# Optimization experiments

Measured on AMD Instinct MI355X. Metric: run time of the kernel, lower is better.

## Reference

```python
import jax, jax.numpy as jnp
import numpy as np

N, E, B = 10000, 160000, 16
IN, H, A, L, OUT = 16, 64, 8, 2, 1
MSG_IN = 2 * (H + 1) + 1   # 131 = concat(x_i, x_j, additional_message_features)
UPD_IN = H + 1 + H         # 129 = concat(x_aug, aggregated message)


def _tp(h, a, W, b):
    # scalar-irreps fully-connected O3 tensor product == bilinear map + bias
    return jnp.einsum('ni,nj,ijk->nk', h, a, W) + b


def setup_inputs() -> dict:
    key = jax.random.key(0)
    ks = jax.random.split(key, 24)
    f32 = jnp.float32
    def rn(k, shape, scale=1.0):
        return jax.random.normal(k, shape, f32) * scale
    def w(k, shape):
        fan = shape[-3] * shape[-2]
        return rn(k, shape, 1.0 / np.sqrt(fan))
    return {
        'x': rn(ks[0], (N, IN)),
        'edge_index': jax.random.randint(ks[1], (2, E), 0, N),
        'edge_attr': rn(ks[2], (E, A)),
        'node_attr': rn(ks[3], (N, A)),
        'additional_message_features': rn(ks[4], (E, 1)),
        'additional_node_features': rn(ks[5], (N, 1)),
        'batch': jnp.sort(jax.random.randint(ks[6], (N,), 0, B)),
        'W_emb': w(ks[7], (IN + 1, A, H)), 'b_emb': jnp.zeros((H,), f32),
        'Wm1': w(ks[8], (L, MSG_IN, A, H)), 'bm1': jnp.zeros((L, H), f32),
        'Wm2': w(ks[9], (L, H, A, H)), 'bm2': jnp.zeros((L, H), f32),
        'Wu1': w(ks[10], (L, UPD_IN, A, H)), 'bu1': jnp.zeros((L, H), f32),
        'Wu2': w(ks[11], (L, H, A, H)), 'bu2': jnp.zeros((L, H), f32),
        'Wp1': w(ks[12], (H, A, H)), 'bp1': jnp.zeros((H,), f32),
        'Wp2': w(ks[13], (H, A, H)), 'bp2': jnp.zeros((H,), f32),
        'Wq1': rn(ks[14], (H, H), 1.0 / np.sqrt(H)), 'bq1': jnp.zeros((H,), f32),
        'Wq2': rn(ks[15], (H, OUT), 1.0 / np.sqrt(H)), 'bq2': jnp.zeros((OUT,), f32),
    }


def _forward(x, edge_attr, node_attr, amf, anf,
             W_emb, b_emb, Wm1, bm1, Wm2, bm2, Wu1, bu1, Wu2, bu2,
             Wp1, bp1, Wp2, bp2, Wq1, bq1, Wq2, bq2, edge_index, batch):
    silu = jax.nn.silu
    src, dst = edge_index[0], edge_index[1]  # source_to_target: aggregate at dst
    n = x.shape[0]
    # embedding: concat additional node features, bilinear TP with node_attr
    h = _tp(jnp.concatenate([x, anf], -1), node_attr, W_emb, b_emb)          # [N,H]
    for l in range(Wm1.shape[0]):  # loop over structurally distinct layers
        h_aug = jnp.concatenate([h, anf], -1)                                # [N,H+1]
        m_in = jnp.concatenate([h_aug[dst], h_aug[src], amf], -1)            # [E,MSG_IN]
        m = silu(_tp(m_in, edge_attr, Wm1[l], bm1[l]))                       # TP + swish gate
        m = silu(_tp(m, edge_attr, Wm2[l], bm2[l]))                          # sg2=True -> gated too
        agg = jax.ops.segment_sum(m, dst, num_segments=n)                    # scatter-add [N,H]
        u = silu(_tp(jnp.concatenate([h_aug, agg], -1), node_attr, Wu1[l], bu1[l]))
        u = _tp(u, node_attr, Wu2[l], bu2[l])                                # no gate on 2nd TP
        h = h + u                                                            # residual, adnid stripped
    # pre-pool MLP (SwishGate TP then plain TP)
    p = silu(_tp(h, node_attr, Wp1, bp1))
    p = _tp(p, node_attr, Wp2, bp2)                                          # [N,POOL=H]
    # global mean pool over graphs
    counts = jax.ops.segment_sum(jnp.ones((n,), p.dtype), batch, num_segments=B)
    g = jax.ops.segment_sum(p, batch, num_segments=B) / jnp.maximum(counts, 1.0)[:, None]
    # post-pool: TP with trivial 1x0e attr == plain linear
    g = silu(g @ Wq1 + bq1)
    return g @ Wq2 + bq2                                                     # [B,OUT]


def reference(x, edge_index, edge_attr, node_attr, additional_message_features,
              additional_node_features, batch, W_emb, b_emb, Wm1, bm1, Wm2, bm2,
              Wu1, bu1, Wu2, bu2, Wp1, bp1, Wp2, bp2, Wq1, bq1, Wq2, bq2):
    return _forward(x, edge_attr, node_attr, additional_message_features,
                    additional_node_features, W_emb, b_emb, Wm1, bm1, Wm2, bm2,
                    Wu1, bu1, Wu2, bu2, Wp1, bp1, Wp2, bp2, Wq1, bq1, Wq2, bq2,
                    edge_index, batch)
```

## Files before the change

kernel.cpp:

```cpp
#include <hip/hip_runtime.h>
#include <hip/hip_bf16.h>
#include <math.h>

constexpr int N = 10000;
constexpr int E = 160000;
constexpr int B = 16;
constexpr int POOL_CHUNKS = 80;
constexpr int MS = 72;
constexpr int HS = 96;

typedef short bf16x8 __attribute__((ext_vector_type(8)));
typedef short bf16x4 __attribute__((ext_vector_type(4)));
typedef float f32x4 __attribute__((ext_vector_type(4)));

__device__ __forceinline__ float silu_f(float x) {
    return x / (1.0f + __expf(-x));
}
__device__ __forceinline__ float bf2f(short s) {
    union { unsigned u; float f; } c; c.u = (unsigned)(unsigned short)s << 16; return c.f;
}

__device__ __forceinline__ void w2_body(
        int idx, const float* __restrict__ Wsrc,
        __hip_bfloat16* __restrict__ Whi, __hip_bfloat16* __restrict__ Wlo) {
    int l = idx >> 15;
    int rem = idx & 32767;
    int kk = rem >> 11;
    int nt = (rem >> 9) & 3;
    int c  = (rem >> 5) & 15;
    int q  = (rem >> 3) & 3;
    int j  = rem & 7;
    int i = q * 16 + kk;
    int k = nt * 16 + c;
    float wv = Wsrc[(size_t)l * 32768 + i * 512 + j * 64 + k];
    __hip_bfloat16 hi = __float2bfloat16(wv);
    Whi[idx] = hi;
    Wlo[idx] = __float2bfloat16(wv - __bfloat162float(hi));
}

__device__ __forceinline__ void w2h_body(
        int idx, const float* __restrict__ Wsrc, __hip_bfloat16* __restrict__ Whi) {
    int l = idx >> 15;
    int rem = idx & 32767;
    int kk = rem >> 11;
    int nt = (rem >> 9) & 3;
    int c  = (rem >> 5) & 15;
    int q  = (rem >> 3) & 3;
    int j  = rem & 7;
    int i = q * 16 + kk;
    int k = nt * 16 + c;
    Whi[idx] = __float2bfloat16(Wsrc[(size_t)l * 32768 + i * 512 + j * 64 + k]);
}

__device__ __forceinline__ void wu1_body(
        int idx, const float* __restrict__ Wu1,
        __hip_bfloat16* __restrict__ Whi, __hip_bfloat16* __restrict__ Wlo) {
    int l = idx / 67584;
    int rem = idx % 67584;
    int kk = rem / 2048;
    int r2 = rem % 2048;
    int nt = (r2 >> 9) & 3;
    int c  = (r2 >> 5) & 15;
    int q  = (r2 >> 3) & 3;
    int j  = r2 & 7;
    int i = q * 33 + kk;
    float wv = (i < 129) ? Wu1[(size_t)l * 129 * 512 + i * 512 + j * 64 + nt * 16 + c] : 0.f;
    __hip_bfloat16 hi = __float2bfloat16(wv);
    Whi[idx] = hi;
    Wlo[idx] = __float2bfloat16(wv - __bfloat162float(hi));
}

__device__ __forceinline__ void wm1z_body(
        int idx, const float* __restrict__ Wm1, __hip_bfloat16* __restrict__ Whi) {
    int l = idx / 71680;
    int rem = idx % 71680;
    int kkn = rem >> 9;
    int off = rem & 511;
    int kk = kkn >> 2;
    int nt = kkn & 3;
    int c16 = off >> 5;
    int q = (off >> 3) & 3;
    int j = off & 7;
    int k = nt * 16 + c16;
    int wi = -1;
    if (kk < 17) { int i = q * 17 + kk; if (i <= 64) wi = i; }
    else if (kk < 34) { int s = q * 17 + (kk - 17); if (s <= 64) wi = 65 + s; }
    else { if (q == 0) wi = 130; }
    float wv = (wi >= 0) ? Wm1[((size_t)l * 131 + wi) * 512 + j * 64 + k] : 0.f;
    Whi[idx] = __float2bfloat16(wv);
}

constexpr int PB_W2H  = 0;
constexpr int PB_WM1Z = PB_W2H  + 256;
constexpr int PB_WU1  = PB_WM1Z + 560;
constexpr int PB_WU2  = PB_WU1  + 528;
constexpr int PB_WP1  = PB_WU2  + 256;
constexpr int PB_WP2  = PB_WP1  + 128;
constexpr int PB_ZERO = PB_WP2  + 128;
constexpr int PB_EMB  = PB_ZERO + 40;
constexpr int PB_TOTAL= PB_EMB  + 625;

__global__ __launch_bounds__(256) void k_pre(
        const float* __restrict__ Wm2, __hip_bfloat16* __restrict__ W2hi,
        const float* __restrict__ Wm1, __hip_bfloat16* __restrict__ Wm1zhi,
        const float* __restrict__ Wu1w, __hip_bfloat16* __restrict__ Wu1hi, __hip_bfloat16* __restrict__ Wu1lo,
        const float* __restrict__ Wu2w, __hip_bfloat16* __restrict__ Wu2hi, __hip_bfloat16* __restrict__ Wu2lo,
        const float* __restrict__ Wp1w, __hip_bfloat16* __restrict__ Wp1hi, __hip_bfloat16* __restrict__ Wp1lo,
        const float* __restrict__ Wp2w, __hip_bfloat16* __restrict__ Wp2hi, __hip_bfloat16* __restrict__ Wp2lo,
        int* __restrict__ hist,
        const float* __restrict__ x, const float* __restrict__ anf,
        const float* __restrict__ na, const float* __restrict__ W_emb,
        const float* __restrict__ b_emb,
        float* __restrict__ h, __hip_bfloat16* __restrict__ hb, float* __restrict__ agg) {
    __shared__ float xs[16][18];
    __shared__ float na_s[16][8];
    int tid = threadIdx.x;
    int bx = blockIdx.x;
    if (bx < PB_WM1Z) {
        w2h_body((bx - PB_W2H) * 256 + tid, Wm2, W2hi);
    } else if (bx < PB_WU1) {
        wm1z_body((bx - PB_WM1Z) * 256 + tid, Wm1, Wm1zhi);
    } else if (bx < PB_WU2) {
        wu1_body((bx - PB_WU1) * 256 + tid, Wu1w, Wu1hi, Wu1lo);
    } else if (bx < PB_WP1) {
        w2_body((bx - PB_WU2) * 256 + tid, Wu2w, Wu2hi, Wu2lo);
    } else if (bx < PB_WP2) {
        w2_body((bx - PB_WP1) * 256 + tid, Wp1w, Wp1hi, Wp1lo);
    } else if (bx < PB_ZERO) {
        w2_body((bx - PB_WP2) * 256 + tid, Wp2w, Wp2hi, Wp2lo);
    } else if (bx < PB_EMB) {
        int i = (bx - PB_ZERO) * 256 + tid;
        if (i < N) hist[i] = 0;
    } else {
        int eb = bx - PB_EMB;
        int w = tid >> 6, l = tid & 63;
        int n0 = eb * 16;
        {
            int r = tid >> 4, c = tid & 15;
            xs[r][c] = x[(size_t)(n0 + r) * 16 + c];
        }
        if (tid < 16) xs[tid][16] = anf[n0 + tid];
        if (tid < 128) na_s[tid >> 3][tid & 7] = na[(size_t)n0 * 8 + tid];
        float4 z4 = {0.f, 0.f, 0.f, 0.f};
        ((float4*)(agg + (size_t)eb * 1024))[tid] = z4;
        for (int t = tid; t < 192; t += 256)
            ((float4*)(hb + (size_t)n0 * HS))[t] = z4;
        __syncthreads();
        float acc[4];
#pragma unroll
        for (int t = 0; t < 4; ++t) acc[t] = b_emb[l];
        for (int i = 0; i < 17; ++i) {
#pragma unroll
            for (int j = 0; j < 8; ++j) {
                float wv = W_emb[(i * 8 + j) * 64 + l];
#pragma unroll
                for (int t = 0; t < 4; ++t) {
                    int nn = w * 4 + t;
                    acc[t] = fmaf(xs[nn][i] * na_s[nn][j], wv, acc[t]);
                }
            }
        }
        int slot = (l / 17) * 24 + l % 17;
#pragma unroll
        for (int t = 0; t < 4; ++t) {
            int n = n0 + w * 4 + t;
            h[(size_t)n * 64 + l] = acc[t];
            hb[(size_t)n * HS + slot] = __float2bfloat16(acc[t]);
        }
        if (tid < 16) hb[(size_t)(n0 + tid) * HS + 85] = __float2bfloat16(xs[tid][16]);
    }
}

__global__ __launch_bounds__(256) void k_hist(
        const int* __restrict__ eidx, int* __restrict__ hist) {
    int e = blockIdx.x * 256 + threadIdx.x;
    if (e < E) atomicAdd(&hist[eidx[E + e]], 1);
}

__global__ __launch_bounds__(1024) void k_scan(
        const int* __restrict__ hist, int* __restrict__ cursor) {
    __shared__ int wsum[16];
    int t = threadIdx.x;
    int base = t * 10;
    int loc[10];
    int s = 0;
#pragma unroll
    for (int i = 0; i < 10; ++i) {
        int v = (base + i < N) ? hist[base + i] : 0;
        loc[i] = s;
        s += v;
    }
    int lane = t & 63, w = t >> 6;
    int incl = s;
    for (int off = 1; off < 64; off <<= 1) {
        int u = __shfl_up(incl, off, 64);
        if (lane >= off) incl += u;
    }
    if (lane == 63) wsum[w] = incl;
    __syncthreads();
    if (t == 0) {
        int a = 0;
        for (int i2 = 0; i2 < 16; ++i2) { int v = wsum[i2]; wsum[i2] = a; a += v; }
    }
    __syncthreads();
    int excl = incl - s + wsum[w];
#pragma unroll
    for (int i = 0; i < 10; ++i) {
        int p = base + i;
        if (p < N) cursor[p] = excl + loc[i];
    }
}

__global__ __launch_bounds__(256) void k_scatter_sort(
        const int* __restrict__ eidx, const float* __restrict__ ea,
        const float* __restrict__ amf, int* __restrict__ cursor,
        int* __restrict__ dstS, float4* __restrict__ recs) {
    int e = blockIdx.x * 256 + threadIdx.x;
    if (e < E) {
        int d = eidx[E + e];
        int p = atomicAdd(&cursor[d], 1);
        dstS[p] = d;
        float4 a0 = ((const float4*)ea)[(size_t)e * 2];
        float4 a1 = ((const float4*)ea)[(size_t)e * 2 + 1];
        float4 r0 = {__int_as_float(eidx[e]), amf[e], a0.x, a0.y};
        float4 r1 = {a0.z, a0.w, a1.x, a1.y};
        float4 r2 = {a1.z, a1.w, 0.f, 0.f};
        recs[(size_t)p * 3 + 0] = r0;
        recs[(size_t)p * 3 + 1] = r1;
        recs[(size_t)p * 3 + 2] = r2;
    }
}

__device__ __forceinline__ void zgemm_stage(
        const __hip_bfloat16* xsrc, int xstride, int kkmax, int Lq,
        int w, int c16, int q, int lofs, const float* naA,
        const __hip_bfloat16* __restrict__ Whi, const __hip_bfloat16* __restrict__ Wlo,
        float (*part_s)[16][64]) {
    f32x4 zero4 = {0.f, 0.f, 0.f, 0.f};
    f32x4 acc[4];
#pragma unroll
    for (int nt = 0; nt < 4; ++nt) acc[nt] = zero4;
    for (int kk = w; kk < kkmax; kk += 4) {
        bf16x8 bh[4], bl[4];
#pragma unroll
        for (int nt = 0; nt < 4; ++nt) {
            int off = (kk * 4 + nt) * 512 + lofs;
            bh[nt] = *(const bf16x8*)(Whi + off);
            bl[nt] = *(const bf16x8*)(Wlo + off);
        }
        float mv = __bfloat162float(xsrc[c16 * xstride + q * Lq + kk]);
        union { bf16x8 v; __hip_bfloat16 hx[8]; } au;
#pragma unroll
        for (int j = 0; j < 8; ++j) au.hx[j] = __float2bfloat16(mv * naA[j]);
#pragma unroll
        for (int nt = 0; nt < 4; ++nt) {
            acc[nt] = __builtin_amdgcn_mfma_f32_16x16x32_bf16(au.v, bh[nt], acc[nt], 0, 0, 0);
            acc[nt] = __builtin_amdgcn_mfma_f32_16x16x32_bf16(au.v, bl[nt], acc[nt], 0, 0, 0);
        }
    }
#pragma unroll
    for (int nt = 0; nt < 4; ++nt)
#pragma unroll
        for (int r = 0; r < 4; ++r) part_s[w][q * 4 + r][nt * 16 + c16] = acc[nt][r];
}

__global__ __launch_bounds__(256, 4) void k_edge(
        const float4* __restrict__ recs, const int* __restrict__ dstS,
        const __hip_bfloat16* __restrict__ hb,
        const __hip_bfloat16* __restrict__ W1hi, const float* __restrict__ bm1_l,
        const __hip_bfloat16* __restrict__ W2hi,
        const float* __restrict__ bm2_l, float* __restrict__ agg) {
    __shared__ __align__(16) char smem_u[4 * 4608];
    __shared__ int dst_s[128];
    int tid = threadIdx.x;
    int l = tid & 63, w = tid >> 6;
    int e0 = blockIdx.x * 128;
    __hip_bfloat16* m_s = (__hip_bfloat16*)(smem_u + w * 4608);
    float* m2 = (float*)(smem_u + w * 4608);

    if (l < 32) dst_s[w * 32 + l] = dstS[e0 + w * 32 + l];

    int c16 = l & 15, q = l >> 4;
    int e0w = w * 32;
    float eaA[2][8], amfA[2];
    int dL[2], sL[2];
#pragma unroll
    for (int mt = 0; mt < 2; ++mt) {
        int e = e0 + e0w + mt * 16 + c16;
        float4 r0 = recs[(size_t)e * 3];
        float4 r1 = recs[(size_t)e * 3 + 1];
        float4 r2 = recs[(size_t)e * 3 + 2];
        sL[mt] = __float_as_int(r0.x);
        amfA[mt] = r0.y;
        eaA[mt][0] = r0.z; eaA[mt][1] = r0.w;
        eaA[mt][2] = r1.x; eaA[mt][3] = r1.y; eaA[mt][4] = r1.z; eaA[mt][5] = r1.w;
        eaA[mt][6] = r2.x; eaA[mt][7] = r2.y;
        dL[mt] = dstS[e];
    }
    float bR1[4], bR2[4];
#pragma unroll
    for (int nt = 0; nt < 4; ++nt) {
        bR1[nt] = bm1_l[nt * 16 + c16];
        bR2[nt] = bm2_l[nt * 16 + c16];
    }
    int lofs = (c16 * 4 + q) * 8;
    f32x4 zero4 = {0.f, 0.f, 0.f, 0.f};

    bf16x4 xD[2][5], xS[2][5];
#pragma unroll
    for (int mt = 0; mt < 2; ++mt) {
        const __hip_bfloat16* bd = hb + (size_t)dL[mt] * HS + q * 24;
        const __hip_bfloat16* bs = hb + (size_t)sL[mt] * HS + q * 24;
#pragma unroll
        for (int t = 0; t < 5; ++t) {
            xD[mt][t] = *(const bf16x4*)(bd + t * 4);
            xS[mt][t] = *(const bf16x4*)(bs + t * 4);
        }
    }

    f32x4 acc1[2][4];
#pragma unroll
    for (int mt = 0; mt < 2; ++mt)
#pragma unroll
        for (int nt = 0; nt < 4; ++nt) acc1[mt][nt] = zero4;
    {
        bf16x8 bhr[3][4];
#pragma unroll
        for (int u = 0; u < 2; ++u)
#pragma unroll
            for (int nt = 0; nt < 4; ++nt)
                bhr[u][nt] = *(const bf16x8*)(W1hi + (u * 4 + nt) * 512 + lofs);
#pragma unroll
        for (int u = 0; u < 35; ++u) {
            if (u + 2 < 35) {
#pragma unroll
                for (int nt = 0; nt < 4; ++nt)
                    bhr[(u + 2) % 3][nt] = *(const bf16x8*)(W1hi + ((u + 2) * 4 + nt) * 512 + lofs);
            }
#pragma unroll
            for (int mt = 0; mt < 2; ++mt) {
                float xv;
                if (u < 17)       xv = bf2f(xD[mt][u >> 2][u & 3]);
                else if (u < 34)  { int s = u - 17; xv = bf2f(xS[mt][s >> 2][s & 3]); }
                else              xv = (q == 0) ? amfA[mt] : 0.f;
                union { bf16x8 v; __hip_bfloat16 hx[8]; } au;
#pragma unroll
                for (int j = 0; j < 8; ++j) au.hx[j] = __float2bfloat16(xv * eaA[mt][j]);
#pragma unroll
                for (int nt = 0; nt < 4; ++nt)
                    acc1[mt][nt] = __builtin_amdgcn_mfma_f32_16x16x32_bf16(au.v, bhr[u % 3][nt], acc1[mt][nt], 0, 0, 0);
            }
            if ((u & 7) == 7 && u < 34) __syncthreads();
        }
    }
#pragma unroll
    for (int mt = 0; mt < 2; ++mt)
#pragma unroll
        for (int nt = 0; nt < 4; ++nt) {
            int kd = nt * 16 + c16;
            float bias = bR1[nt];
#pragma unroll
            for (int r = 0; r < 4; ++r) {
                int el = mt * 16 + q * 4 + r;
                m_s[el * MS + kd] = __float2bfloat16(silu_f(bias + acc1[mt][nt][r]));
            }
        }

    bf16x4 mR[2][4];
#pragma unroll
    for (int mt = 0; mt < 2; ++mt)
#pragma unroll
        for (int t = 0; t < 4; ++t)
            mR[mt][t] = *(const bf16x4*)&m_s[(mt * 16 + c16) * MS + q * 16 + t * 4];

    asm volatile("" ::: "memory");

    f32x4 acc[2][4];
#pragma unroll
    for (int mt = 0; mt < 2; ++mt)
#pragma unroll
        for (int nt = 0; nt < 4; ++nt) acc[mt][nt] = zero4;
    {
        bf16x8 bhr[3][4];
#pragma unroll
        for (int u = 0; u < 2; ++u)
#pragma unroll
            for (int nt = 0; nt < 4; ++nt)
                bhr[u][nt] = *(const bf16x8*)(W2hi + (u * 4 + nt) * 512 + lofs);
#pragma unroll
        for (int kk = 0; kk < 16; ++kk) {
            if (kk + 2 < 16) {
#pragma unroll
                for (int nt = 0; nt < 4; ++nt)
                    bhr[(kk + 2) % 3][nt] = *(const bf16x8*)(W2hi + ((kk + 2) * 4 + nt) * 512 + lofs);
            }
#pragma unroll
            for (int mt = 0; mt < 2; ++mt) {
                float mv = bf2f(mR[mt][kk >> 2][kk & 3]);
                union { bf16x8 v; __hip_bfloat16 h[8]; } au;
#pragma unroll
                for (int j = 0; j < 8; ++j) au.h[j] = __float2bfloat16(mv * eaA[mt][j]);
#pragma unroll
                for (int nt = 0; nt < 4; ++nt)
                    acc[mt][nt] = __builtin_amdgcn_mfma_f32_16x16x32_bf16(au.v, bhr[kk % 3][nt], acc[mt][nt], 0, 0, 0);
            }
            if (kk == 7) __syncthreads();
        }
    }

#pragma unroll
    for (int mt = 0; mt < 2; ++mt) {
#pragma unroll
        for (int nt = 0; nt < 4; ++nt) {
            int kd = nt * 16 + c16;
            float bias = bR2[nt];
#pragma unroll
            for (int r = 0; r < 4; ++r)
                m2[(q * 4 + r) * 66 + kd] = silu_f(bias + acc[mt][nt][r]);
        }
        int rb = w * 32 + mt * 16;
        float run = 0.f;
        int cur_d = dst_s[rb];
        for (int i = 0; i < 16; ++i) {
            int d = dst_s[rb + i];
            if (d != cur_d) {
                atomicAdd(&agg[(size_t)cur_d * 64 + l], run);
                run = 0.f;
                cur_d = d;
            }
            run += m2[i * 66 + l];
        }
        atomicAdd(&agg[(size_t)cur_d * 64 + l], run);
        asm volatile("" ::: "memory");
    }
}

__global__ __launch_bounds__(256) void k_upd_hb(
        const float* __restrict__ h_in, const float* __restrict__ anf,
        const float* __restrict__ na, const float* __restrict__ agg_in,
        const __hip_bfloat16* __restrict__ W1hi, const __hip_bfloat16* __restrict__ W1lo,
        const float* __restrict__ bu1_l,
        const __hip_bfloat16* __restrict__ W2hi_, const __hip_bfloat16* __restrict__ W2lo_,
        const float* __restrict__ bu2_l,
        float* __restrict__ h, __hip_bfloat16* __restrict__ hb, float* __restrict__ agg) {
    __shared__ __align__(16) __hip_bfloat16 xa_s[16 * 136];
    __shared__ __align__(16) __hip_bfloat16 u1_s[16 * 72];
    __shared__ float part_s[4][16][64];
    int tid = threadIdx.x;
    int w = tid >> 6, l = tid & 63;
    int n0 = blockIdx.x * 16;
    for (int idx = tid; idx < 16 * 132; idx += 256) {
        int r = idx / 132, c = idx % 132;
        int n = n0 + r;
        float v;
        if (c < 64) v = h_in[(size_t)n * 64 + c];
        else if (c == 64) v = anf[n];
        else if (c < 129) v = agg_in[(size_t)n * 64 + (c - 65)];
        else v = 0.f;
        xa_s[r * 136 + c] = __float2bfloat16(v);
    }
    int c16 = l & 15, q = l >> 4;
    float naA[8];
#pragma unroll
    for (int j = 0; j < 8; ++j) naA[j] = na[(size_t)(n0 + c16) * 8 + j];
    __syncthreads();
    float4 z4 = {0.f, 0.f, 0.f, 0.f};
    ((float4*)(agg + (size_t)blockIdx.x * 1024))[tid] = z4;
    for (int t = tid; t < 192; t += 256)
        ((float4*)(hb + (size_t)n0 * HS))[t] = z4;
    int lofs = (c16 * 4 + q) * 8;
    zgemm_stage(xa_s, 136, 33, 33, w, c16, q, lofs, naA, W1hi, W1lo, part_s);
    __syncthreads();
    for (int t = tid; t < 1024; t += 256) {
        int row = t >> 6, col = t & 63;
        float v = part_s[0][row][col] + part_s[1][row][col] + part_s[2][row][col] +
                  part_s[3][row][col] + bu1_l[col];
        u1_s[row * 72 + col] = __float2bfloat16(silu_f(v));
    }
    __syncthreads();
    zgemm_stage(u1_s, 72, 16, 16, w, c16, q, lofs, naA, W2hi_, W2lo_, part_s);
    __syncthreads();
    for (int t = tid; t < 1024; t += 256) {
        int row = t >> 6, col = t & 63;
        float v = part_s[0][row][col] + part_s[1][row][col] + part_s[2][row][col] +
                  part_s[3][row][col] + bu2_l[col];
        int n = n0 + row;
        float hn = h[(size_t)n * 64 + col] + v;
        h[(size_t)n * 64 + col] = hn;
        hb[(size_t)n * HS + (col / 17) * 24 + col % 17] = __float2bfloat16(hn);
    }
    if (tid < 16) hb[(size_t)(n0 + tid) * HS + 85] = __float2bfloat16(anf[n0 + tid]);
}

__global__ __launch_bounds__(256) void k_upd_prepool(
        const float* __restrict__ h_in, const float* __restrict__ anf,
        const float* __restrict__ na, const float* __restrict__ agg_in,
        const __hip_bfloat16* __restrict__ W1hi, const __hip_bfloat16* __restrict__ W1lo,
        const float* __restrict__ bu1_l,
        const __hip_bfloat16* __restrict__ W2hi_, const __hip_bfloat16* __restrict__ W2lo_,
        const float* __restrict__ bu2_l,
        const __hip_bfloat16* __restrict__ Wp1hi, const __hip_bfloat16* __restrict__ Wp1lo,
        const float* __restrict__ bp1,
        const __hip_bfloat16* __restrict__ Wp2hi, const __hip_bfloat16* __restrict__ Wp2lo,
        const float* __restrict__ bp2,
        float* __restrict__ p2) {
    __shared__ __align__(16) __hip_bfloat16 xa_s[16 * 136];
    __shared__ __align__(16) __hip_bfloat16 u1_s[16 * 72];
    __shared__ __align__(16) __hip_bfloat16 x2_s[16 * 72];
    __shared__ float part_s[4][16][64];
    int tid = threadIdx.x;
    int w = tid >> 6, l = tid & 63;
    int n0 = blockIdx.x * 16;
    for (int idx = tid; idx < 16 * 132; idx += 256) {
        int r = idx / 132, c = idx % 132;
        int n = n0 + r;
        float v;
        if (c < 64) v = h_in[(size_t)n * 64 + c];
        else if (c == 64) v = anf[n];
        else if (c < 129) v = agg_in[(size_t)n * 64 + (c - 65)];
        else v = 0.f;
        xa_s[r * 136 + c] = __float2bfloat16(v);
    }
    int c16 = l & 15, q = l >> 4;
    float naA[8];
#pragma unroll
    for (int j = 0; j < 8; ++j) naA[j] = na[(size_t)(n0 + c16) * 8 + j];
    __syncthreads();
    int lofs = (c16 * 4 + q) * 8;
    zgemm_stage(xa_s, 136, 33, 33, w, c16, q, lofs, naA, W1hi, W1lo, part_s);
    __syncthreads();
    for (int t = tid; t < 1024; t += 256) {
        int row = t >> 6, col = t & 63;
        float v = part_s[0][row][col] + part_s[1][row][col] + part_s[2][row][col] +
                  part_s[3][row][col] + bu1_l[col];
        u1_s[row * 72 + col] = __float2bfloat16(silu_f(v));
    }
    __syncthreads();
    zgemm_stage(u1_s, 72, 16, 16, w, c16, q, lofs, naA, W2hi_, W2lo_, part_s);
    __syncthreads();
    for (int t = tid; t < 1024; t += 256) {
        int row = t >> 6, col = t & 63;
        float v = part_s[0][row][col] + part_s[1][row][col] + part_s[2][row][col] +
                  part_s[3][row][col] + bu2_l[col];
        float hn = h_in[(size_t)(n0 + row) * 64 + col] + v;
        x2_s[row * 72 + col] = __float2bfloat16(hn);
    }
    __syncthreads();
    zgemm_stage(x2_s, 72, 16, 16, w, c16, q, lofs, naA, Wp1hi, Wp1lo, part_s);
    __syncthreads();
    for (int t = tid; t < 1024; t += 256) {
        int row = t >> 6, col = t & 63;
        float v = part_s[0][row][col] + part_s[1][row][col] + part_s[2][row][col] +
                  part_s[3][row][col] + bp1[col];
        u1_s[row * 72 + col] = __float2bfloat16(silu_f(v));
    }
    __syncthreads();
    zgemm_stage(u1_s, 72, 16, 16, w, c16, q, lofs, naA, Wp2hi, Wp2lo, part_s);
    __syncthreads();
    for (int t = tid; t < 1024; t += 256) {
        int row = t >> 6, col = t & 63;
        float v = part_s[0][row][col] + part_s[1][row][col] + part_s[2][row][col] +
                  part_s[3][row][col] + bp2[col];
        p2[(size_t)(n0 + row) * 64 + col] = v;
    }
}

__global__ __launch_bounds__(256) void k_pool(
        const float* __restrict__ p2, const int* __restrict__ batch,
        float* __restrict__ partial_p, float* __restrict__ partial_cnt) {
    __shared__ float acc_s[16 * 64];
    __shared__ float cnt_s[16];
    int tid = threadIdx.x;
    for (int idx = tid; idx < 1024; idx += 256) acc_s[idx] = 0.f;
    if (tid < 16) cnt_s[tid] = 0.f;
    __syncthreads();
    int w = tid >> 6, k = tid & 63;
    int base = blockIdx.x * 125;
    for (int i = 0; i < 32; ++i) {
        int nl = i * 4 + w;
        if (nl < 125) {
            int n = base + nl;
            int b = batch[n];
            atomicAdd(&acc_s[b * 64 + k], p2[(size_t)n * 64 + k]);
            if (k == 0) atomicAdd(&cnt_s[b], 1.0f);
        }
    }
    __syncthreads();
    for (int idx = tid; idx < 1024; idx += 256)
        partial_p[(size_t)blockIdx.x * 1024 + idx] = acc_s[idx];
    if (tid < 16) partial_cnt[blockIdx.x * 16 + tid] = cnt_s[tid];
}

__global__ __launch_bounds__(1024) void k_final(
        const float* __restrict__ partial_p, const float* __restrict__ partial_cnt,
        const float* __restrict__ Wq1, const float* __restrict__ bq1,
        const float* __restrict__ Wq2, const float* __restrict__ bq2,
        float* __restrict__ out) {
    __shared__ float g[16][64];
    int b = threadIdx.x >> 6, k = threadIdx.x & 63;
    float s = 0.f, cc = 0.f;
    for (int c = 0; c < POOL_CHUNKS; ++c) s += partial_p[(size_t)c * 1024 + b * 64 + k];
    for (int c = 0; c < POOL_CHUNKS; ++c) cc += partial_cnt[c * 16 + b];
    g[b][k] = s / fmaxf(cc, 1.0f);
    __syncthreads();
    float acc = bq1[k];
#pragma unroll
    for (int i = 0; i < 64; ++i) acc = fmaf(g[b][i], Wq1[i * 64 + k], acc);
    float v = silu_f(acc) * Wq2[k];
#pragma unroll
    for (int off = 32; off > 0; off >>= 1) v += __shfl_down(v, off, 64);
    if (k == 0) out[b] = v + bq2[0];
}

extern "C" void kernel_launch(void* const* d_in, const int* in_sizes, int n_in,
                              void* d_out, int out_size, void* d_ws, size_t ws_size,
                              hipStream_t stream) {
    const float* x    = (const float*)d_in[0];
    const int*   eidx = (const int*)  d_in[1];
    const float* ea   = (const float*)d_in[2];
    const float* na   = (const float*)d_in[3];
    const float* amf  = (const float*)d_in[4];
    const float* anf  = (const float*)d_in[5];
    const int*   batch= (const int*)  d_in[6];
    const float* W_emb= (const float*)d_in[7];
    const float* b_emb= (const float*)d_in[8];
    const float* Wm1  = (const float*)d_in[9];
    const float* bm1  = (const float*)d_in[10];
    const float* Wm2  = (const float*)d_in[11];
    const float* bm2  = (const float*)d_in[12];
    const float* Wu1  = (const float*)d_in[13];
    const float* bu1  = (const float*)d_in[14];
    const float* Wu2  = (const float*)d_in[15];
    const float* bu2  = (const float*)d_in[16];
    const float* Wp1  = (const float*)d_in[17];
    const float* bp1  = (const float*)d_in[18];
    const float* Wp2  = (const float*)d_in[19];
    const float* bp2  = (const float*)d_in[20];
    const float* Wq1  = (const float*)d_in[21];
    const float* bq1  = (const float*)d_in[22];
    const float* Wq2  = (const float*)d_in[23];
    const float* bq2  = (const float*)d_in[24];

    float* ws = (float*)d_ws;
    float* h      = ws;
    float* agg    = h + (size_t)N * 64;
    float* p2     = agg + (size_t)N * 64;
    float* part_p = p2 + (size_t)N * 64;
    float* part_c = part_p + POOL_CHUNKS * 1024;
    float* fend   = part_c + POOL_CHUNKS * 16;
    __hip_bfloat16* hb     = (__hip_bfloat16*)fend;
    __hip_bfloat16* W2hi   = hb + (size_t)N * HS;
    __hip_bfloat16* Wm1zhi = W2hi + 65536;
    __hip_bfloat16* Wu1hi  = Wm1zhi + 143360;
    __hip_bfloat16* Wu1lo  = Wu1hi + 135168;
    __hip_bfloat16* Wu2hi  = Wu1lo + 135168;
    __hip_bfloat16* Wu2lo  = Wu2hi + 65536;
    __hip_bfloat16* Wp1hi  = Wu2lo + 65536;
    __hip_bfloat16* Wp1lo  = Wp1hi + 32768;
    __hip_bfloat16* Wp2hi  = Wp1lo + 32768;
    __hip_bfloat16* Wp2lo  = Wp2hi + 32768;
    int* hist   = (int*)(Wp2lo + 32768);
    int* cursor = hist + N;
    int* dstS   = cursor + N;
    float4* recs = (float4*)(dstS + E);

    k_pre<<<PB_TOTAL, 256, 0, stream>>>(
        Wm2, W2hi, Wm1, Wm1zhi, Wu1, Wu1hi, Wu1lo, Wu2, Wu2hi, Wu2lo,
        Wp1, Wp1hi, Wp1lo, Wp2, Wp2hi, Wp2lo, hist,
        x, anf, na, W_emb, b_emb, h, hb, agg);

    k_hist<<<(E + 255) / 256, 256, 0, stream>>>(eidx, hist);
    k_scan<<<1, 1024, 0, stream>>>(hist, cursor);
    k_scatter_sort<<<(E + 255) / 256, 256, 0, stream>>>(eidx, ea, amf, cursor, dstS, recs);

    k_edge<<<E / 128, 256, 0, stream>>>(recs, dstS, hb,
                                        Wm1zhi, bm1, W2hi, bm2, agg);
    k_upd_hb<<<625, 256, 0, stream>>>(h, anf, na, agg,
                                      Wu1hi, Wu1lo, bu1,
                                      Wu2hi, Wu2lo, bu2,
                                      h, hb, agg);
    k_edge<<<E / 128, 256, 0, stream>>>(recs, dstS, hb,
                                        Wm1zhi + 71680, bm1 + 64,
                                        W2hi + 32768, bm2 + 64, agg);
    k_upd_prepool<<<625, 256, 0, stream>>>(h, anf, na, agg,
                                           Wu1hi + 67584, Wu1lo + 67584, bu1 + 64,
                                           Wu2hi + 32768, Wu2lo + 32768, bu2 + 64,
                                           Wp1hi, Wp1lo, bp1, Wp2hi, Wp2lo, bp2, p2);
    k_pool<<<POOL_CHUNKS, 256, 0, stream>>>(p2, batch, part_p, part_c);
    k_final<<<1, 1024, 0, stream>>>(part_p, part_c, Wq1, bq1, Wq2, bq2, (float*)d_out);
}
```

Measured before the change: 388.6 us.

## Stage edge-MLP weights through double-buffered LDS instead of per-wave global loads

Stages both message-MLP weight matrices into a double-buffered 32 KB shared-memory tile that the whole block loads cooperatively, one 4-k-step chunk at a time, with the next chunk prefetched into registers while the current one is used. Previously each wave streamed the weights from global/L2 through a 3-deep register ring. The aim is to cut redundant global weight traffic across the four waves and to merge the two GEMM phases into one pipelined loop. In exchange the kernel adds a barrier per chunk, uses far more LDS, and lowers launch_bounds occupancy from 4 to 3 blocks per CU.

```diff
diff --git a/kernel.cpp b/kernel.cpp
--- a/kernel.cpp
+++ b/kernel.cpp
@@ -264,12 +264,13 @@
         for (int r = 0; r < 4; ++r) part_s[w][q * 4 + r][nt * 16 + c16] = acc[nt][r];
 }
 
-__global__ __launch_bounds__(256, 4) void k_edge(
+__global__ __launch_bounds__(256, 3) void k_edge(
         const float4* __restrict__ recs, const int* __restrict__ dstS,
         const __hip_bfloat16* __restrict__ hb,
         const __hip_bfloat16* __restrict__ W1hi, const float* __restrict__ bm1_l,
         const __hip_bfloat16* __restrict__ W2hi,
         const float* __restrict__ bm2_l, float* __restrict__ agg) {
+    __shared__ __align__(16) __hip_bfloat16 wbuf[2][8192];
     __shared__ __align__(16) char smem_u[4 * 4608];
     __shared__ int dst_s[128];
     int tid = threadIdx.x;
@@ -318,93 +319,105 @@
         }
     }
 
-    f32x4 acc1[2][4];
+    {
+#pragma unroll
+        for (int r = 0; r < 4; ++r) {
+            float4 v = ((const float4*)W1hi)[r * 256 + tid];
+            ((float4*)wbuf[0])[r * 256 + tid] = v;
+        }
+    }
+
+    f32x4 acc1[2][4], acc2[2][4];
 #pragma unroll
     for (int mt = 0; mt < 2; ++mt)
 #pragma unroll
-        for (int nt = 0; nt < 4; ++nt) acc1[mt][nt] = zero4;
-    {
-        bf16x8 bhr[3][4];
-#pragma unroll
-        for (int u = 0; u < 2; ++u)
-#pragma unroll
-            for (int nt = 0; nt < 4; ++nt)
-                bhr[u][nt] = *(const bf16x8*)(W1hi + (u * 4 + nt) * 512 + lofs);
-#pragma unroll
-        for (int u = 0; u < 35; ++u) {
-            if (u + 2 < 35) {
+        for (int nt = 0; nt < 4; ++nt) { acc1[mt][nt] = zero4; acc2[mt][nt] = zero4; }
+    bf16x4 mR[2][4];
+
+#pragma unroll
+    for (int c = 0; c < 13; ++c) {
+        __syncthreads();
+        float4 lv[4];
+        if (c + 1 < 13) {
+            const __hip_bfloat16* nsrc = (c + 1 < 9) ? (W1hi + (c + 1) * 8192)
+                                                     : (W2hi + (c + 1 - 9) * 8192);
+            const int nk = (c + 1 == 8) ? 3 : 4;
+#pragma unroll
+            for (int r = 0; r < 4; ++r)
+                if (r < nk) lv[r] = ((const float4*)nsrc)[r * 256 + tid];
+        }
+        const __hip_bfloat16* wb = wbuf[c & 1];
+        if (c < 9) {
+            const int nkk = (c == 8) ? 3 : 4;
+#pragma unroll
+            for (int kkl = 0; kkl < 4; ++kkl) {
+                if (kkl < nkk) {
+                    const int u = c * 4 + kkl;
+                    bf16x8 bh[4];
+#pragma unroll
+                    for (int nt = 0; nt < 4; ++nt)
+                        bh[nt] = *(const bf16x8*)&wb[(kkl * 4 + nt) * 512 + lofs];
+#pragma unroll
+                    for (int mt = 0; mt < 2; ++mt) {
+                        float xv;
+                        if (u < 17)      xv = bf2f(xD[mt][u >> 2][u & 3]);
+                        else if (u < 34) { const int s = u - 17; xv = bf2f(xS[mt][s >> 2][s & 3]); }
+                        else             xv = (q == 0) ? amfA[mt] : 0.f;
+                        union { bf16x8 v; __hip_bfloat16 hx[8]; } au;
+#pragma unroll
+                        for (int j = 0; j < 8; ++j) au.hx[j] = __float2bfloat16(xv * eaA[mt][j]);
+#pragma unroll
+                        for (int nt = 0; nt < 4; ++nt)
+                            acc1[mt][nt] = __builtin_amdgcn_mfma_f32_16x16x32_bf16(au.v, bh[nt], acc1[mt][nt], 0, 0, 0);
+                    }
+                }
+            }
+        } else {
+#pragma unroll
+            for (int kkl = 0; kkl < 4; ++kkl) {
+                const int kk = (c - 9) * 4 + kkl;
+                bf16x8 bh[4];
 #pragma unroll
                 for (int nt = 0; nt < 4; ++nt)
-                    bhr[(u + 2) % 3][nt] = *(const bf16x8*)(W1hi + ((u + 2) * 4 + nt) * 512 + lofs);
+                    bh[nt] = *(const bf16x8*)&wb[(kkl * 4 + nt) * 512 + lofs];
+#pragma unroll
+                for (int mt = 0; mt < 2; ++mt) {
+                    float mv = bf2f(mR[mt][kk >> 2][kk & 3]);
+                    union { bf16x8 v; __hip_bfloat16 hx[8]; } au;
+#pragma unroll
+                    for (int j = 0; j < 8; ++j) au.hx[j] = __float2bfloat16(mv * eaA[mt][j]);
+#pragma unroll
+                    for (int nt = 0; nt < 4; ++nt)
+                        acc2[mt][nt] = __builtin_amdgcn_mfma_f32_16x16x32_bf16(au.v, bh[nt], acc2[mt][nt], 0, 0, 0);
+                }
             }
-#pragma unroll
-            for (int mt = 0; mt < 2; ++mt) {
-                float xv;
-                if (u < 17)       xv = bf2f(xD[mt][u >> 2][u & 3]);
-                else if (u < 34)  { int s = u - 17; xv = bf2f(xS[mt][s >> 2][s & 3]); }
-                else              xv = (q == 0) ? amfA[mt] : 0.f;
-                union { bf16x8 v; __hip_bfloat16 hx[8]; } au;
-#pragma unroll
-                for (int j = 0; j < 8; ++j) au.hx[j] = __float2bfloat16(xv * eaA[mt][j]);
-#pragma unroll
-                for (int nt = 0; nt < 4; ++nt)
-                    acc1[mt][nt] = __builtin_amdgcn_mfma_f32_16x16x32_bf16(au.v, bhr[u % 3][nt], acc1[mt][nt], 0, 0, 0);
-            }
-            if ((u & 7) == 7 && u < 34) __syncthreads();
-        }
-    }
-#pragma unroll
-    for (int mt = 0; mt < 2; ++mt)
-#pragma unroll
-        for (int nt = 0; nt < 4; ++nt) {
-            int kd = nt * 16 + c16;
-            float bias = bR1[nt];
-#pragma unroll
-            for (int r = 0; r < 4; ++r) {
-                int el = mt * 16 + q * 4 + r;
-                m_s[el * MS + kd] = __float2bfloat16(silu_f(bias + acc1[mt][nt][r]));
-            }
-        }
-
-    bf16x4 mR[2][4];
-#pragma unroll
-    for (int mt = 0; mt < 2; ++mt)
-#pragma unroll
-        for (int t = 0; t < 4; ++t)
-            mR[mt][t] = *(const bf16x4*)&m_s[(mt * 16 + c16) * MS + q * 16 + t * 4];
-
-    asm volatile("" ::: "memory");
-
-    f32x4 acc[2][4];
-#pragma unroll
-    for (int mt = 0; mt < 2; ++mt)
-#pragma unroll
-        for (int nt = 0; nt < 4; ++nt) acc[mt][nt] = zero4;
-    {
-        bf16x8 bhr[3][4];
-#pragma unroll
-        for (int u = 0; u < 2; ++u)
-#pragma unroll
-            for (int nt = 0; nt < 4; ++nt)
-                bhr[u][nt] = *(const bf16x8*)(W2hi + (u * 4 + nt) * 512 + lofs);
-#pragma unroll
-        for (int kk = 0; kk < 16; ++kk) {
-            if (kk + 2 < 16) {
-#pragma unroll
-                for (int nt = 0; nt < 4; ++nt)
-                    bhr[(kk + 2) % 3][nt] = *(const bf16x8*)(W2hi + ((kk + 2) * 4 + nt) * 512 + lofs);
-            }
-#pragma unroll
-            for (int mt = 0; mt < 2; ++mt) {
-                float mv = bf2f(mR[mt][kk >> 2][kk & 3]);
-                union { bf16x8 v; __hip_bfloat16 h[8]; } au;
-#pragma unroll
-                for (int j = 0; j < 8; ++j) au.h[j] = __float2bfloat16(mv * eaA[mt][j]);
-#pragma unroll
-                for (int nt = 0; nt < 4; ++nt)
-                    acc[mt][nt] = __builtin_amdgcn_mfma_f32_16x16x32_bf16(au.v, bhr[kk % 3][nt], acc[mt][nt], 0, 0, 0);
-            }
-            if (kk == 7) __syncthreads();
+        }
+        if (c == 8) {
+#pragma unroll
+            for (int mt = 0; mt < 2; ++mt)
+#pragma unroll
+                for (int nt = 0; nt < 4; ++nt) {
+                    int kd = nt * 16 + c16;
+                    float bias = bR1[nt];
+#pragma unroll
+                    for (int r = 0; r < 4; ++r) {
+                        int el = mt * 16 + q * 4 + r;
+                        m_s[el * MS + kd] = __float2bfloat16(silu_f(bias + acc1[mt][nt][r]));
+                    }
+                }
+#pragma unroll
+            for (int mt = 0; mt < 2; ++mt)
+#pragma unroll
+                for (int t = 0; t < 4; ++t)
+                    mR[mt][t] = *(const bf16x4*)&m_s[(mt * 16 + c16) * MS + q * 16 + t * 4];
+            asm volatile("" ::: "memory");
+        }
+        if (c + 1 < 13) {
+            const int nk = (c + 1 == 8) ? 3 : 4;
+            float4* wdst = (float4*)wbuf[(c + 1) & 1];
+#pragma unroll
+            for (int r = 0; r < 4; ++r)
+                if (r < nk) wdst[r * 256 + tid] = lv[r];
         }
     }
 
@@ -416,7 +429,7 @@
             float bias = bR2[nt];
 #pragma unroll
             for (int r = 0; r < 4; ++r)
-                m2[(q * 4 + r) * 66 + kd] = silu_f(bias + acc[mt][nt][r]);
+                m2[(q * 4 + r) * 66 + kd] = silu_f(bias + acc2[mt][nt][r]);
         }
         int rb = w * 32 + mt * 16;
         float run = 0.f;
```

New measurement: 373.2 us. -3.9%, faster.
